# Kernel tuning notes

Measured on AMD Instinct MI355X. Metric: run time of the kernel, lower is better.

Reference implementation:

```python
import jax, jax.numpy as jnp
import numpy as np

N = 16          # automaton states
M = 64          # predicates
R = 2           # clauses per edge
B = 4096        # batch
E = N * N       # edges
LIT_TEMP = 0.8
ROW_TEMP = 0.5

def _build_mask():
    mask = np.full((N, N), -np.inf, dtype=np.float32)
    for q in range(N):
        mask[q, q] = 0.0
        mask[q, (q + 1) % N] = 0.0
    return jnp.asarray(mask)

def setup_inputs() -> dict:
    key = jax.random.key(0)
    k1, k2, k3 = jax.random.split(key, 3)
    u_t = jax.random.uniform(k1, (B, M), dtype=jnp.float32)
    # stacked per-edge parameters (original has n*n separate DNFEdge modules)
    sel = 0.5 * jax.random.normal(k2, (E, R, M, 3), dtype=jnp.float32)
    alog = 0.5 * jax.random.normal(k3, (E, R), dtype=jnp.float32)
    mask = _build_mask()  # [N, N], 0 on allowed edges, -inf elsewhere
    return {"u_t": u_t, "sel": sel, "alog": alog, "mask": mask}

def reference(u_t, sel, alog, mask):
    # DNFEdge.forward, batched over all E = n*n edges at once
    selector = jax.nn.softmax(sel / max(LIT_TEMP, 1e-6), axis=-1)     # [E,R,M,3]
    u = u_t[:, None, None, :]                                          # [B,1,1,M]
    L = (selector[None, ..., 0]
         + selector[None, ..., 1] * u
         + selector[None, ..., 2] * (1.0 - u))                         # [B,E,R,M]
    C = jnp.clip(L, 0.0, 1.0).prod(axis=-1)                            # [B,E,R]
    alpha = jax.nn.sigmoid(alog)[None]                                 # [1,E,R]
    z = jnp.clip(alpha * C, 0.0, 1.0)
    g = 1.0 - (1.0 - z).prod(axis=-1)                                  # [B,E]
    G = g.reshape(B, N, N)
    logits = jnp.log(jnp.clip(G, 1e-6, None)) + mask                   # [B,N,N]
    # row fallback: if a row has no finite entry, force self-loop
    row_has_finite = jnp.isfinite(logits).any(axis=-1, keepdims=True)
    eye = jnp.eye(N, dtype=logits.dtype)
    logits = jnp.where(row_has_finite, logits, 10.0 * eye)
    return jax.nn.softmax(logits / max(ROW_TEMP, 1e-6), axis=-1).astype(jnp.float32)
```

## Files before the change

kernel.cpp:

```cpp
#include <hip/hip_runtime.h>


#define AB_STRIDE 260
#define U_STRIDE  68

__global__ __launch_bounds__(512) void fused_kernel(
    const float* __restrict__ u_t, const float* __restrict__ sel,
    const float* __restrict__ alog, float* __restrict__ out) {
  __shared__ float ab4[32 * AB_STRIDE];
  __shared__ float u_s[16 * U_STRIDE];
  __shared__ float alpha_s[64];
  __shared__ float gs[16][33];
  __shared__ float ps[16][33];

  const int tid = threadIdx.x;
  const int bid = blockIdx.x;

  #pragma unroll
  for (int k = 0; k < 8; ++k) {
    int idx = k * 512 + tid;
    int m  = idx & 63;
    int r  = (idx >> 6) & 1;
    int ke = idx >> 7;
    int q   = ke >> 1;
    int col = (q + (ke & 1)) & 15;
    int e   = q * 16 + col;
    const float* s = sel + ((size_t)((e * 2 + r) * 64 + m)) * 3;
    float s0 = s[0] * 1.25f, s1 = s[1] * 1.25f, s2 = s[2] * 1.25f;
    float mx = fmaxf(s0, fmaxf(s1, s2));
    float e0 = __expf(s0 - mx), e1 = __expf(s1 - mx), e2 = __expf(s2 - mx);
    float inv = 1.0f / (e0 + e1 + e2);
    float a = (e0 + e2) * inv;
    float b = (e1 - e2) * inv;
    float2* dst = (float2*)&ab4[ke * AB_STRIDE + m * 4 + r * 2];
    *dst = make_float2(a, b);
  }

  if (tid < 64) {
    int ke = tid >> 1, r = tid & 1;
    int q = ke >> 1, col = (q + (ke & 1)) & 15;
    int e = q * 16 + col;
    float a = alog[e * 2 + r];
    alpha_s[tid] = 1.0f / (1.0f + __expf(-a));
  }

  if (tid < 256) {
    int row = tid >> 4, j = tid & 15;
    float4 v = *(const float4*)(u_t + (size_t)bid * 1024 + row * 64 + j * 4);
    *(float4*)&u_s[row * U_STRIDE + j * 4] = v;
  }
  __syncthreads();

  const int ke = tid >> 4;
  const int lb = tid & 15;
  const float* uu    = &u_s[lb * U_STRIDE];
  const float* abrow = &ab4[ke * AB_STRIDE];

  float C0 = 1.0f, C1 = 1.0f;
  #pragma unroll 8
  for (int m = 0; m < 64; ++m) {
    float4 w = *(const float4*)(abrow + m * 4);
    float u  = uu[m];
    float L0 = fmaf(w.y, u, w.x);
    float L1 = fmaf(w.w, u, w.z);
    L0 = fminf(fmaxf(L0, 0.0f), 1.0f);
    L1 = fminf(fmaxf(L1, 0.0f), 1.0f);
    C0 *= L0;
    C1 *= L1;
  }
  float z0 = alpha_s[ke * 2]     * C0;
  float z1 = alpha_s[ke * 2 + 1] * C1;
  z0 = fminf(fmaxf(z0, 0.0f), 1.0f);
  z1 = fminf(fmaxf(z1, 0.0f), 1.0f);
  float g  = 1.0f - (1.0f - z0) * (1.0f - z1);
  float Gc = fmaxf(g, 1e-6f);
  gs[lb][ke] = Gc;
  __syncthreads();

  float Go = gs[lb][ke ^ 1];
  float x2 = Gc * Gc, y2 = Go * Go;
  ps[lb][ke] = x2 / (x2 + y2);
  __syncthreads();

  float4* obase = (float4*)(out + (size_t)bid * 4096);
  #pragma unroll
  for (int j = 0; j < 2; ++j) {
    int fidx = j * 512 + tid;
    int bl   = fidx >> 6;
    int rem  = fidx & 63;
    int q    = rem >> 2;
    int c0   = (rem & 3) * 4;
    int nq   = (q + 1) & 15;
    float4 v;
    float* vp = (float*)&v;
    #pragma unroll
    for (int c = 0; c < 4; ++c) {
      int col = c0 + c;
      float x = 0.0f;
      if (col == q)       x = ps[bl][2 * q];
      else if (col == nq) x = ps[bl][2 * q + 1];
      vp[c] = x;
    }
    obase[fidx] = v;
  }
}

extern "C" void kernel_launch(void* const* d_in, const int* in_sizes, int n_in,
                              void* d_out, int out_size, void* d_ws, size_t ws_size,
                              hipStream_t stream) {
  const float* u_t  = (const float*)d_in[0];
  const float* sel  = (const float*)d_in[1];
  const float* alog = (const float*)d_in[2];
  float* out = (float*)d_out;
  fused_kernel<<<256, 512, 0, stream>>>(u_t, sel, alog, out);
}
```

Before: 10.11 us.

## Split predicate product across thread pairs with 1024-thread blocks and shuffles

Doubles the block size to 1024 threads and splits each thread's 64-predicate clause product into two halves across lane pairs, combining them with a warp shuffle. The cross-edge normalization now uses a shuffle instead of a shared-memory round trip, which removes one barrier. The softmax over selectors drops the max subtraction and uses the hardware reciprocal. Dropping the max shift risks overflow only for large selector values, and the reciprocal is approximate; the larger block raises register pressure limits and per-block sync cost.

```diff
diff --git a/kernel.cpp b/kernel.cpp
--- a/kernel.cpp
+++ b/kernel.cpp
@@ -2,106 +2,100 @@
 
 
 #define AB_STRIDE 260
-#define U_STRIDE  68
+#define U_STRIDE  65
 
-__global__ __launch_bounds__(512) void fused_kernel(
+__global__ __launch_bounds__(1024) void fused_kernel(
     const float* __restrict__ u_t, const float* __restrict__ sel,
     const float* __restrict__ alog, float* __restrict__ out) {
   __shared__ float ab4[32 * AB_STRIDE];
   __shared__ float u_s[16 * U_STRIDE];
   __shared__ float alpha_s[64];
-  __shared__ float gs[16][33];
   __shared__ float ps[16][33];
 
   const int tid = threadIdx.x;
   const int bid = blockIdx.x;
 
+  {
+    float v = u_t[(size_t)bid * 1024 + tid];
+    int row = tid >> 6, j = tid & 63;
+    u_s[row * U_STRIDE + j] = v;
+  }
+
   #pragma unroll
-  for (int k = 0; k < 8; ++k) {
-    int idx = k * 512 + tid;
+  for (int k = 0; k < 4; ++k) {
+    int idx = k * 1024 + tid;
     int m  = idx & 63;
     int r  = (idx >> 6) & 1;
     int ke = idx >> 7;
     int q   = ke >> 1;
     int col = (q + (ke & 1)) & 15;
     int e   = q * 16 + col;
-    const float* s = sel + ((size_t)((e * 2 + r) * 64 + m)) * 3;
-    float s0 = s[0] * 1.25f, s1 = s[1] * 1.25f, s2 = s[2] * 1.25f;
-    float mx = fmaxf(s0, fmaxf(s1, s2));
-    float e0 = __expf(s0 - mx), e1 = __expf(s1 - mx), e2 = __expf(s2 - mx);
-    float inv = 1.0f / (e0 + e1 + e2);
+    const float* s = sel + (size_t)((e * 2 + r) * 64 + m) * 3;
+    float e0 = __expf(s[0] * 1.25f);
+    float e1 = __expf(s[1] * 1.25f);
+    float e2 = __expf(s[2] * 1.25f);
+    float inv = __builtin_amdgcn_rcpf(e0 + e1 + e2);
     float a = (e0 + e2) * inv;
     float b = (e1 - e2) * inv;
-    float2* dst = (float2*)&ab4[ke * AB_STRIDE + m * 4 + r * 2];
-    *dst = make_float2(a, b);
+    *(float2*)&ab4[ke * AB_STRIDE + m * 4 + r * 2] = make_float2(a, b);
   }
 
   if (tid < 64) {
     int ke = tid >> 1, r = tid & 1;
     int q = ke >> 1, col = (q + (ke & 1)) & 15;
     int e = q * 16 + col;
-    float a = alog[e * 2 + r];
-    alpha_s[tid] = 1.0f / (1.0f + __expf(-a));
-  }
-
-  if (tid < 256) {
-    int row = tid >> 4, j = tid & 15;
-    float4 v = *(const float4*)(u_t + (size_t)bid * 1024 + row * 64 + j * 4);
-    *(float4*)&u_s[row * U_STRIDE + j * 4] = v;
+    alpha_s[tid] = __builtin_amdgcn_rcpf(1.0f + __expf(-alog[e * 2 + r]));
   }
   __syncthreads();
 
-  const int ke = tid >> 4;
-  const int lb = tid & 15;
-  const float* uu    = &u_s[lb * U_STRIDE];
-  const float* abrow = &ab4[ke * AB_STRIDE];
+  const int half = tid & 1;
+  const int lb   = (tid >> 1) & 15;
+  const int ke   = tid >> 5;
+  const float* uu    = &u_s[lb * U_STRIDE + half * 32];
+  const float* abrow = &ab4[ke * AB_STRIDE + half * 128];
 
-  float C0 = 1.0f, C1 = 1.0f;
-  #pragma unroll 8
-  for (int m = 0; m < 64; ++m) {
-    float4 w = *(const float4*)(abrow + m * 4);
-    float u  = uu[m];
-    float L0 = fmaf(w.y, u, w.x);
-    float L1 = fmaf(w.w, u, w.z);
-    L0 = fminf(fmaxf(L0, 0.0f), 1.0f);
-    L1 = fminf(fmaxf(L1, 0.0f), 1.0f);
-    C0 *= L0;
-    C1 *= L1;
+  float c0a = 1.0f, c0b = 1.0f, c1a = 1.0f, c1b = 1.0f;
+  #pragma unroll
+  for (int i = 0; i < 32; i += 2) {
+    float4 w0 = *(const float4*)(abrow + i * 4);
+    float4 w1 = *(const float4*)(abrow + i * 4 + 4);
+    float ua = uu[i], ub = uu[i + 1];
+    c0a *= fminf(fmaxf(fmaf(w0.y, ua, w0.x), 0.0f), 1.0f);
+    c1a *= fminf(fmaxf(fmaf(w0.w, ua, w0.z), 0.0f), 1.0f);
+    c0b *= fminf(fmaxf(fmaf(w1.y, ub, w1.x), 0.0f), 1.0f);
+    c1b *= fminf(fmaxf(fmaf(w1.w, ub, w1.z), 0.0f), 1.0f);
   }
-  float z0 = alpha_s[ke * 2]     * C0;
-  float z1 = alpha_s[ke * 2 + 1] * C1;
-  z0 = fminf(fmaxf(z0, 0.0f), 1.0f);
-  z1 = fminf(fmaxf(z1, 0.0f), 1.0f);
+  float C0 = c0a * c0b, C1 = c1a * c1b;
+  float o0 = __shfl_xor(C0, 1, 64);
+  float o1 = __shfl_xor(C1, 1, 64);
+  C0 *= o0;
+  C1 *= o1;
+
+  float z0 = fminf(fmaxf(alpha_s[ke * 2]     * C0, 0.0f), 1.0f);
+  float z1 = fminf(fmaxf(alpha_s[ke * 2 + 1] * C1, 0.0f), 1.0f);
   float g  = 1.0f - (1.0f - z0) * (1.0f - z1);
   float Gc = fmaxf(g, 1e-6f);
-  gs[lb][ke] = Gc;
+  float Go = __shfl_xor(Gc, 32, 64);
+  float x2 = Gc * Gc, y2 = Go * Go;
+  float p  = x2 * __builtin_amdgcn_rcpf(x2 + y2);
+  if (half == 0) ps[lb][ke] = p;
   __syncthreads();
 
-  float Go = gs[lb][ke ^ 1];
-  float x2 = Gc * Gc, y2 = Go * Go;
-  ps[lb][ke] = x2 / (x2 + y2);
-  __syncthreads();
-
-  float4* obase = (float4*)(out + (size_t)bid * 4096);
-  #pragma unroll
-  for (int j = 0; j < 2; ++j) {
-    int fidx = j * 512 + tid;
-    int bl   = fidx >> 6;
-    int rem  = fidx & 63;
-    int q    = rem >> 2;
-    int c0   = (rem & 3) * 4;
-    int nq   = (q + 1) & 15;
+  {
+    int bl  = tid >> 6;
+    int rem = tid & 63;
+    int q   = rem >> 2;
+    int c0  = (rem & 3) * 4;
+    int nq  = (q + 1) & 15;
+    float pd = ps[bl][2 * q], pn = ps[bl][2 * q + 1];
     float4 v;
     float* vp = (float*)&v;
     #pragma unroll
     for (int c = 0; c < 4; ++c) {
       int col = c0 + c;
-      float x = 0.0f;
-      if (col == q)       x = ps[bl][2 * q];
-      else if (col == nq) x = ps[bl][2 * q + 1];
-      vp[c] = x;
+      vp[c] = (col == q) ? pd : (col == nq) ? pn : 0.0f;
     }
-    obase[fidx] = v;
+    ((float4*)(out + (size_t)bid * 4096))[tid] = v;
   }
 }
 
@@ -112,5 +106,5 @@
   const float* sel  = (const float*)d_in[1];
   const float* alog = (const float*)d_in[2];
   float* out = (float*)d_out;
-  fused_kernel<<<256, 512, 0, stream>>>(u_t, sel, alog, out);
+  fused_kernel<<<256, 1024, 0, stream>>>(u_t, sel, alog, out);
 }
```

Measured after the change: 10.99 us. 8.7% more time.
